# Kernel optimization log

Hardware: AMD Instinct MI355X
Metric: run time of the kernel (lower is better)

The kernel has to match this reference:

```python
import jax, jax.numpy as jnp
import numpy as np

N = 50000
E = 800000
IN_FEATS = 256
HIDDEN = 512
N_CLASSES = 40


def setup_inputs() -> dict:
    key = jax.random.key(0)
    ks = jax.random.split(key, 12)
    x = jax.random.normal(ks[0], (N, IN_FEATS), dtype=jnp.float32)
    src = jax.random.randint(ks[1], (E,), 0, N, dtype=jnp.int32)
    dst = jax.random.randint(ks[2], (E,), 0, N, dtype=jnp.int32)
    def glorot(k, fan_in, fan_out):
        lim = jnp.sqrt(6.0 / (fan_in + fan_out)).astype(jnp.float32)
        return jax.random.uniform(k, (fan_in, fan_out), jnp.float32, -lim, lim)
    W1 = glorot(ks[3], IN_FEATS, HIDDEN); b1 = jnp.zeros((HIDDEN,), jnp.float32)
    W2 = glorot(ks[4], HIDDEN, HIDDEN);   b2 = jnp.zeros((HIDDEN,), jnp.float32)
    W3 = glorot(ks[5], HIDDEN, HIDDEN);   b3 = jnp.zeros((HIDDEN,), jnp.float32)
    W4 = glorot(ks[6], HIDDEN, N_CLASSES); b4 = jnp.zeros((N_CLASSES,), jnp.float32)
    return {"x": x, "src": src, "dst": dst,
            "W1": W1, "b1": b1, "W2": W2, "b2": b2,
            "W3": W3, "b3": b3, "W4": W4, "b4": b4}


def _deg_inv_sqrt(idx, n):
    deg = jax.ops.segment_sum(jnp.ones_like(idx, jnp.float32), idx, num_segments=n)
    return jnp.where(deg > 0, jax.lax.rsqrt(jnp.maximum(deg, 1.0)), 0.0)


def _graph_conv(h, W, b, src, dst, c_src, c_dst, activation):
    # DGL GraphConv, norm='both': out = D_in^{-1/2} A D_out^{-1/2} h W + b
    h = h @ W                      # [N, out] dense transform first (reduces edge traffic)
    m = (h * c_src[:, None])[src]  # [E, out] gathered, src-normalized messages
    agg = jax.ops.segment_sum(m, dst, num_segments=h.shape[0])  # [N, out]
    out = agg * c_dst[:, None] + b
    return activation(out) if activation is not None else out


def reference(x, src, dst, W1, b1, W2, b2, W3, b3, W4, b4):
    n = x.shape[0]
    c_src = _deg_inv_sqrt(src, n)  # out-degree^{-1/2}
    c_dst = _deg_inv_sqrt(dst, n)  # in-degree^{-1/2}
    h = _graph_conv(x, W1, b1, src, dst, c_src, c_dst, jax.nn.relu)
    h = _graph_conv(h, W2, b2, src, dst, c_src, c_dst, jax.nn.relu)
    # dropout is identity in eval mode
    h = _graph_conv(h, W3, b3, src, dst, c_src, c_dst, jax.nn.relu)
    h = _graph_conv(h, W4, b4, src, dst, c_src, c_dst, None)
    return h
```

## Files before the change

### kernel.cpp

```cpp
#include <hip/hip_runtime.h>
#include <hip/hip_bf16.h>


#define GCN_N 50000
#define GCN_E 800000

typedef unsigned short u16;
typedef __attribute__((ext_vector_type(4))) float f32x4;
typedef __attribute__((ext_vector_type(4))) _Float16 f16x4;
typedef __attribute__((ext_vector_type(8))) _Float16 f16x8;

__device__ __forceinline__ void gload_lds16(const void* g, void* l) {
  __builtin_amdgcn_global_load_lds((const __attribute__((address_space(1))) void*)g,
                                   (__attribute__((address_space(3))) void*)l, 16, 0, 0);
}


__global__ void hist_kernel(const int* __restrict__ src, const int* __restrict__ dst,
                            int* __restrict__ deg_src, int* __restrict__ deg_dst, int E) {
  int i = blockIdx.x * blockDim.x + threadIdx.x;
  if (i < E) {
    atomicAdd(&deg_src[src[i]], 1);
    atomicAdd(&deg_dst[dst[i]], 1);
  }
}

__global__ void cinv_kernel(const int* __restrict__ deg_src, const int* __restrict__ deg_dst,
                            float* __restrict__ c_src, float* __restrict__ c_dst, int n) {
  int i = blockIdx.x * blockDim.x + threadIdx.x;
  if (i < n) {
    int ds = deg_src[i];
    int dd = deg_dst[i];
    c_src[i] = ds > 0 ? 1.0f / sqrtf((float)ds) : 0.0f;
    c_dst[i] = dd > 0 ? 1.0f / sqrtf((float)dd) : 0.0f;
  }
}

__global__ void scan_kernel(const int* __restrict__ deg, int* __restrict__ row_ptr,
                            int* __restrict__ cursor, int n) {
  __shared__ int wsum[16];
  __shared__ int s_carry;
  int lane = threadIdx.x & 63;
  int wid = threadIdx.x >> 6;
  if (threadIdx.x == 0) s_carry = 0;
  __syncthreads();
  for (int base = 0; base < n; base += 1024) {
    int i = base + (int)threadIdx.x;
    int v = (i < n) ? deg[i] : 0;
    int x = v;
    #pragma unroll
    for (int off = 1; off < 64; off <<= 1) {
      int y = __shfl_up(x, off, 64);
      if (lane >= off) x += y;
    }
    if (lane == 63) wsum[wid] = x;
    __syncthreads();
    int woff = s_carry;
    for (int w = 0; w < wid; ++w) woff += wsum[w];
    int incl = woff + x;
    if (i < n) {
      row_ptr[i] = incl - v;
      cursor[i] = incl - v;
    }
    __syncthreads();
    if (threadIdx.x == 1023) s_carry = incl;
    __syncthreads();
  }
  if (threadIdx.x == 0) row_ptr[n] = s_carry;
}

__global__ void fill_csr_kernel(const int* __restrict__ src, const int* __restrict__ dst,
                                int* __restrict__ cursor, int* __restrict__ csr_src, int E) {
  int i = blockIdx.x * blockDim.x + threadIdx.x;
  if (i < E) {
    int slot = atomicAdd(&cursor[dst[i]], 1);
    csr_src[slot] = src[i];
  }
}


__global__ void f32_to_f16_kernel(const float* __restrict__ in, _Float16* __restrict__ out,
                                  long n4) {
  long i = (long)blockIdx.x * blockDim.x + threadIdx.x;
  long stride = (long)gridDim.x * blockDim.x;
  for (; i < n4; i += stride) {
    float4 v = ((const float4*)in)[i];
    f16x4 h;
    h.x = (_Float16)v.x; h.y = (_Float16)v.y; h.z = (_Float16)v.z; h.w = (_Float16)v.w;
    ((f16x4*)out)[i] = h;
  }
}

template <typename VT, int NE, int G>
__global__ void agg16_kernel(const _Float16* __restrict__ in, _Float16* __restrict__ out,
                             const int* __restrict__ row_ptr, const int* __restrict__ csr_src,
                             const float* __restrict__ c_src, const float* __restrict__ c_dst) {
  int d = blockIdx.x;
  int t = threadIdx.x;
  if (t >= G) return;
  int beg = row_ptr[d];
  int end = row_ptr[d + 1];
  const VT* inv = (const VT*)in;
  float acc[NE];
  #pragma unroll
  for (int e = 0; e < NE; ++e) acc[e] = 0.f;
  int s_cur = 0; float c_cur = 0.f;
  if (beg < end) { s_cur = csr_src[beg]; c_cur = c_src[s_cur]; }
  for (int k = beg; k < end; ++k) {
    int s_nxt = 0; float c_nxt = 0.f;
    if (k + 1 < end) { s_nxt = csr_src[k + 1]; c_nxt = c_src[s_nxt]; }
    VT v = inv[(size_t)s_cur * G + t];
    #pragma unroll
    for (int e = 0; e < NE; ++e) acc[e] = fmaf(c_cur, (float)v[e], acc[e]);
    s_cur = s_nxt; c_cur = c_nxt;
  }
  float cd = c_dst[d];
  VT o;
  #pragma unroll
  for (int e = 0; e < NE; ++e) o[e] = (_Float16)(acc[e] * cd);
  ((VT*)out)[(size_t)d * G + t] = o;
}

__global__ void agg40_kernel(const _Float16* __restrict__ in, float* __restrict__ out,
                             const int* __restrict__ row_ptr, const int* __restrict__ csr_src,
                             const float* __restrict__ c_src, const float* __restrict__ c_dst,
                             const float* __restrict__ bias) {
  int d = blockIdx.x;
  int t = threadIdx.x;
  if (t >= 10) return;
  int beg = row_ptr[d];
  int end = row_ptr[d + 1];
  const f16x4* in4 = (const f16x4*)in;
  float ax = 0.f, ay = 0.f, az = 0.f, aw = 0.f;
  int s_cur = 0; float c_cur = 0.f;
  if (beg < end) { s_cur = csr_src[beg]; c_cur = c_src[s_cur]; }
  for (int k = beg; k < end; ++k) {
    int s_nxt = 0; float c_nxt = 0.f;
    if (k + 1 < end) { s_nxt = csr_src[k + 1]; c_nxt = c_src[s_nxt]; }
    f16x4 v = in4[(size_t)s_cur * 10 + t];
    ax = fmaf(c_cur, (float)v.x, ax);
    ay = fmaf(c_cur, (float)v.y, ay);
    az = fmaf(c_cur, (float)v.z, az);
    aw = fmaf(c_cur, (float)v.w, aw);
    s_cur = s_nxt; c_cur = c_nxt;
  }
  float cd = c_dst[d];
  float4 b = ((const float4*)bias)[t];
  float4 o;
  o.x = ax * cd + b.x;
  o.y = ay * cd + b.y;
  o.z = az * cd + b.z;
  o.w = aw * cd + b.w;
  ((float4*)out)[(size_t)d * 10 + t] = o;
}


__global__ void prep_weight_kernel(const float* __restrict__ W, _Float16* __restrict__ th,
                                   _Float16* __restrict__ tl, int K, int N) {
  __shared__ float tile[32][33];
  int bn = blockIdx.x * 32, bk = blockIdx.y * 32;
  int tx = threadIdx.x, ty = threadIdx.y;
  #pragma unroll
  for (int i = 0; i < 4; ++i)
    tile[ty + i * 8][tx] = W[(size_t)(bk + ty + i * 8) * N + bn + tx];
  __syncthreads();
  #pragma unroll
  for (int i = 0; i < 4; ++i) {
    float v = tile[tx][ty + i * 8];
    _Float16 h = (_Float16)v;
    _Float16 l = (_Float16)((v - (float)h) * 4096.f);
    size_t o = (size_t)(bn + ty + i * 8) * K + bk + tx;
    th[o] = h;
    tl[o] = l;
  }
}

__global__ __launch_bounds__(512, 4) void mfma_gemm_kernel(
    const _Float16* __restrict__ A,
    const _Float16* __restrict__ Bh, const _Float16* __restrict__ Bl,
    const float* __restrict__ bias, _Float16* __restrict__ C,
    int M, int K, int N) {
  __shared__ _Float16 sA[128 * 32], sBh[128 * 32], sBl[128 * 32];
  int t = threadIdx.x;
  int lane = t & 63, wid = t >> 6;
  int wr = wid >> 2, wc = wid & 3;
  int lr = lane & 15, ko = lane >> 4;
  int swz = (lr & 3) ^ ((lr >> 2) & 3);
  int koff = ((ko ^ swz) << 3);
  int bm = blockIdx.x * 128, bn = blockIdx.y * 128;

  f32x4 acch[4][2] = {};
  f32x4 accl[4][2] = {};

  int aoff[4], boff[2];
  #pragma unroll
  for (int i = 0; i < 4; ++i) aoff[i] = (wr * 64 + i * 16 + lr) * 32 + koff;
  #pragma unroll
  for (int j = 0; j < 2; ++j) boff[j] = (wc * 32 + j * 16 + lr) * 32 + koff;

  int srow = t >> 2;
  int sc = (t & 3) ^ ((srow & 3) ^ ((srow >> 2) & 3));
  int ldst = wid * 512;
  int gra = bm + srow;
  if (gra >= M) gra = M - 1;
  size_t gabase = (size_t)gra * K + sc * 8;
  size_t gbbase = (size_t)(bn + srow) * K + sc * 8;

  for (int k0 = 0; k0 < K; k0 += 32) {
    gload_lds16(A + gabase + k0, sA + ldst);
    gload_lds16(Bh + gbbase + k0, sBh + ldst);
    gload_lds16(Bl + gbbase + k0, sBl + ldst);
    __syncthreads();
    f16x8 a[4], bh[2], bl[2];
    #pragma unroll
    for (int i = 0; i < 4; ++i) a[i] = *(const f16x8*)(sA + aoff[i]);
    #pragma unroll
    for (int j = 0; j < 2; ++j) {
      bh[j] = *(const f16x8*)(sBh + boff[j]);
      bl[j] = *(const f16x8*)(sBl + boff[j]);
    }
    #pragma unroll
    for (int i = 0; i < 4; ++i)
      #pragma unroll
      for (int j = 0; j < 2; ++j) {
        acch[i][j] = __builtin_amdgcn_mfma_f32_16x16x32_f16(a[i], bh[j], acch[i][j], 0, 0, 0);
        accl[i][j] = __builtin_amdgcn_mfma_f32_16x16x32_f16(a[i], bl[j], accl[i][j], 0, 0, 0);
      }
    __syncthreads();
  }

  const float inv_s = 1.0f / 4096.0f;
  int r0 = (lane >> 4) << 2;
  #pragma unroll
  for (int i = 0; i < 4; ++i) {
    #pragma unroll
    for (int j = 0; j < 2; ++j) {
      int col = bn + wc * 32 + j * 16 + lr;
      float bv = bias[col];
      #pragma unroll
      for (int r = 0; r < 4; ++r) {
        int row = bm + wr * 64 + i * 16 + r0 + r;
        if (row < M) {
          float v = acch[i][j][r] + accl[i][j][r] * inv_s + bv;
          v = v > 0.f ? v : 0.f;
          C[(size_t)row * N + col] = (_Float16)v;
        }
      }
    }
  }
}


__global__ __launch_bounds__(256) void gemm40_kernel(const _Float16* __restrict__ A,
                                                     const float* __restrict__ W,
                                                     _Float16* __restrict__ C,
                                                     int M, int K, int N) {
  __shared__ float As[16][128 + 4];
  __shared__ float Bs[16][128 + 4];
  int tid = threadIdx.x;
  int tx = tid & 15;
  int ty = tid >> 4;
  int bm = blockIdx.x * 128;
  int bn = blockIdx.y * 128;

  float acc[8][8];
  #pragma unroll
  for (int i = 0; i < 8; ++i)
    #pragma unroll
    for (int j = 0; j < 8; ++j) acc[i][j] = 0.f;

  int ar = tid >> 2;
  int akq = (tid & 3) << 2;
  int bkk = tid >> 4;
  int bcq = (tid & 15) << 2;

  for (int k0 = 0; k0 < K; k0 += 16) {
    #pragma unroll
    for (int half = 0; half < 2; ++half) {
      int r = ar + half * 64;
      int grow = bm + r;
      float4 v = make_float4(0.f, 0.f, 0.f, 0.f);
      if (grow < M) {
        f16x4 hv = *(const f16x4*)&A[(size_t)grow * K + k0 + akq];
        v = make_float4((float)hv.x, (float)hv.y, (float)hv.z, (float)hv.w);
      }
      As[akq + 0][r] = v.x;
      As[akq + 1][r] = v.y;
      As[akq + 2][r] = v.z;
      As[akq + 3][r] = v.w;
    }
    #pragma unroll
    for (int half = 0; half < 2; ++half) {
      int c = bcq + half * 64;
      int gc = bn + c;
      float4 v = make_float4(0.f, 0.f, 0.f, 0.f);
      if (gc + 3 < N) v = *(const float4*)&W[(size_t)(k0 + bkk) * N + gc];
      *(float4*)&Bs[bkk][c] = v;
    }
    __syncthreads();
    #pragma unroll
    for (int kk = 0; kk < 16; ++kk) {
      float4 a0 = *(const float4*)&As[kk][ty * 4];
      float4 a1 = *(const float4*)&As[kk][ty * 4 + 64];
      float4 b0 = *(const float4*)&Bs[kk][tx * 4];
      float4 b1 = *(const float4*)&Bs[kk][tx * 4 + 64];
      float a[8] = {a0.x, a0.y, a0.z, a0.w, a1.x, a1.y, a1.z, a1.w};
      float b[8] = {b0.x, b0.y, b0.z, b0.w, b1.x, b1.y, b1.z, b1.w};
      #pragma unroll
      for (int i = 0; i < 8; ++i)
        #pragma unroll
        for (int j = 0; j < 8; ++j) acc[i][j] = fmaf(a[i], b[j], acc[i][j]);
    }
    __syncthreads();
  }

  #pragma unroll
  for (int i = 0; i < 8; ++i) {
    int r = bm + (i < 4 ? ty * 4 + i : 64 + ty * 4 + (i - 4));
    if (r >= M) continue;
    #pragma unroll
    for (int j = 0; j < 8; ++j) {
      int c = bn + (j < 4 ? tx * 4 + j : 64 + tx * 4 + (j - 4));
      if (c >= N) continue;
      C[(size_t)r * N + c] = (_Float16)acc[i][j];
    }
  }
}


extern "C" void kernel_launch(void* const* d_in, const int* in_sizes, int n_in,
                              void* d_out, int out_size, void* d_ws, size_t ws_size,
                              hipStream_t stream) {
  const float* x  = (const float*)d_in[0];
  const int* src  = (const int*)d_in[1];
  const int* dst  = (const int*)d_in[2];
  const float* W1 = (const float*)d_in[3];
  const float* b1 = (const float*)d_in[4];
  const float* W2 = (const float*)d_in[5];
  const float* b2 = (const float*)d_in[6];
  const float* W3 = (const float*)d_in[7];
  const float* b3 = (const float*)d_in[8];
  const float* W4 = (const float*)d_in[9];
  const float* b4 = (const float*)d_in[10];
  float* out = (float*)d_out;

  const int N = GCN_N, E = GCN_E;

  char* ws = (char*)d_ws;
  size_t off = 0;
  _Float16* h16a = (_Float16*)(ws + off); off += (size_t)N * 512 * 2;
  _Float16* h16b = (_Float16*)(ws + off); off += (size_t)N * 512 * 2;
  _Float16* x16  = (_Float16*)(ws + off); off += (size_t)N * 256 * 2;
  float* c_src = (float*)(ws + off); off += (size_t)N * 4;
  float* c_dst = (float*)(ws + off); off += (size_t)N * 4;
  int* row_ptr = (int*)(ws + off); off += (size_t)(N + 4) * 4;
  int* csr_src = (int*)(ws + off); off += (size_t)E * 4;
  _Float16* WtH1 = (_Float16*)(ws + off); off += (size_t)512 * 256 * 2;
  _Float16* WtL1 = (_Float16*)(ws + off); off += (size_t)512 * 256 * 2;
  _Float16* WtH2 = (_Float16*)(ws + off); off += (size_t)512 * 512 * 2;
  _Float16* WtL2 = (_Float16*)(ws + off); off += (size_t)512 * 512 * 2;
  _Float16* WtH3 = (_Float16*)(ws + off); off += (size_t)512 * 512 * 2;
  _Float16* WtL3 = (_Float16*)(ws + off); off += (size_t)512 * 512 * 2;
  int* deg_src = (int*)h16a;
  int* deg_dst = deg_src + N;
  int* cursor  = deg_dst + N;
  _Float16* t4 = x16;

  hipMemsetAsync(deg_src, 0, (size_t)2 * N * 4, stream);
  hist_kernel<<<(E + 255) / 256, 256, 0, stream>>>(src, dst, deg_src, deg_dst, E);
  cinv_kernel<<<(N + 255) / 256, 256, 0, stream>>>(deg_src, deg_dst, c_src, c_dst, N);
  scan_kernel<<<1, 1024, 0, stream>>>(deg_dst, row_ptr, cursor, N);
  fill_csr_kernel<<<(E + 255) / 256, 256, 0, stream>>>(src, dst, cursor, csr_src, E);

  prep_weight_kernel<<<dim3(16, 8), dim3(32, 8), 0, stream>>>(W1, WtH1, WtL1, 256, 512);
  prep_weight_kernel<<<dim3(16, 16), dim3(32, 8), 0, stream>>>(W2, WtH2, WtL2, 512, 512);
  prep_weight_kernel<<<dim3(16, 16), dim3(32, 8), 0, stream>>>(W3, WtH3, WtL3, 512, 512);

  f32_to_f16_kernel<<<2048, 256, 0, stream>>>(x, x16, (long)N * 256 / 4);

  int gm = (N + 127) / 128;

  agg16_kernel<f16x4, 4, 64><<<N, 64, 0, stream>>>(x16, h16a, row_ptr, csr_src, c_src, c_dst);
  mfma_gemm_kernel<<<dim3(gm, 4), 512, 0, stream>>>(h16a, WtH1, WtL1, b1, h16b, N, 256, 512);
  agg16_kernel<f16x8, 8, 64><<<N, 64, 0, stream>>>(h16b, h16a, row_ptr, csr_src, c_src, c_dst);
  mfma_gemm_kernel<<<dim3(gm, 4), 512, 0, stream>>>(h16a, WtH2, WtL2, b2, h16b, N, 512, 512);
  agg16_kernel<f16x8, 8, 64><<<N, 64, 0, stream>>>(h16b, h16a, row_ptr, csr_src, c_src, c_dst);
  mfma_gemm_kernel<<<dim3(gm, 4), 512, 0, stream>>>(h16a, WtH3, WtL3, b3, h16b, N, 512, 512);
  gemm40_kernel<<<dim3(gm, 1), 256, 0, stream>>>(h16b, W4, t4, N, 512, 40);
  agg40_kernel<<<N, 64, 0, stream>>>(t4, out, row_ptr, csr_src, c_src, c_dst, b4);
}
```

Before: 961.9 us.

## Parallelize CSR prefix scan across blocks and deepen gather prefetch in aggregation

Replaces the single-block 1024-thread serial-chunk scan over 50k degrees with a three-kernel reduce/scan/downsweep over 196 blocks, cutting a long serial prologue kernel. The aggregation kernels now prefetch two neighbor feature rows ahead instead of only the next index, keeping more gather loads in flight per thread. This adds two extra kernel launches and extra registers in the aggregation loops.

```diff
diff --git a/kernel.cpp b/kernel.cpp
--- a/kernel.cpp
+++ b/kernel.cpp
@@ -36,37 +36,57 @@
   }
 }
 
-__global__ void scan_kernel(const int* __restrict__ deg, int* __restrict__ row_ptr,
-                            int* __restrict__ cursor, int n) {
-  __shared__ int wsum[16];
-  __shared__ int s_carry;
+__device__ __forceinline__ int block_incl_scan(int v, int* lds) {
   int lane = threadIdx.x & 63;
   int wid = threadIdx.x >> 6;
-  if (threadIdx.x == 0) s_carry = 0;
+  int x = v;
+  #pragma unroll
+  for (int o = 1; o < 64; o <<= 1) {
+    int y = __shfl_up(x, o, 64);
+    if (lane >= o) x += y;
+  }
+  if (lane == 63) lds[wid] = x;
   __syncthreads();
-  for (int base = 0; base < n; base += 1024) {
-    int i = base + (int)threadIdx.x;
-    int v = (i < n) ? deg[i] : 0;
-    int x = v;
-    #pragma unroll
-    for (int off = 1; off < 64; off <<= 1) {
-      int y = __shfl_up(x, off, 64);
-      if (lane >= off) x += y;
-    }
-    if (lane == 63) wsum[wid] = x;
-    __syncthreads();
-    int woff = s_carry;
-    for (int w = 0; w < wid; ++w) woff += wsum[w];
-    int incl = woff + x;
-    if (i < n) {
-      row_ptr[i] = incl - v;
-      cursor[i] = incl - v;
-    }
-    __syncthreads();
-    if (threadIdx.x == 1023) s_carry = incl;
-    __syncthreads();
-  }
-  if (threadIdx.x == 0) row_ptr[n] = s_carry;
+  int off = 0;
+  #pragma unroll
+  for (int w = 0; w < 4; ++w)
+    if (w < wid) off += lds[w];
+  return x + off;
+}
+
+__global__ void deg_partial_kernel(const int* __restrict__ deg, int* __restrict__ partials, int n) {
+  __shared__ int lds[4];
+  int i = blockIdx.x * 256 + threadIdx.x;
+  int v = (i < n) ? deg[i] : 0;
+  int x = v;
+  #pragma unroll
+  for (int o = 1; o < 64; o <<= 1) x += __shfl_xor(x, o, 64);
+  if ((threadIdx.x & 63) == 0) lds[threadIdx.x >> 6] = x;
+  __syncthreads();
+  if (threadIdx.x == 0) partials[blockIdx.x] = lds[0] + lds[1] + lds[2] + lds[3];
+}
+
+__global__ void scan_partials_kernel(int* __restrict__ partials, int* __restrict__ row_ptr,
+                                     int nb, int n) {
+  __shared__ int lds[4];
+  int t = threadIdx.x;
+  int v = (t < nb) ? partials[t] : 0;
+  int incl = block_incl_scan(v, lds);
+  if (t < nb) partials[t] = incl - v;
+  if (t == 255) row_ptr[n] = incl;
+}
+
+__global__ void final_scan_kernel(const int* __restrict__ deg, const int* __restrict__ partials,
+                                  int* __restrict__ row_ptr, int* __restrict__ cursor, int n) {
+  __shared__ int lds[4];
+  int i = blockIdx.x * 256 + threadIdx.x;
+  int v = (i < n) ? deg[i] : 0;
+  int incl = block_incl_scan(v, lds);
+  int excl = incl - v + partials[blockIdx.x];
+  if (i < n) {
+    row_ptr[i] = excl;
+    cursor[i] = excl;
+  }
 }
 
 __global__ void fill_csr_kernel(const int* __restrict__ src, const int* __restrict__ dst,
@@ -99,20 +119,24 @@
   int t = threadIdx.x;
   if (t >= G) return;
   int beg = row_ptr[d];
-  int end = row_ptr[d + 1];
+  int cnt = row_ptr[d + 1] - beg;
   const VT* inv = (const VT*)in;
   float acc[NE];
   #pragma unroll
   for (int e = 0; e < NE; ++e) acc[e] = 0.f;
-  int s_cur = 0; float c_cur = 0.f;
-  if (beg < end) { s_cur = csr_src[beg]; c_cur = c_src[s_cur]; }
-  for (int k = beg; k < end; ++k) {
-    int s_nxt = 0; float c_nxt = 0.f;
-    if (k + 1 < end) { s_nxt = csr_src[k + 1]; c_nxt = c_src[s_nxt]; }
-    VT v = inv[(size_t)s_cur * G + t];
-    #pragma unroll
-    for (int e = 0; e < NE; ++e) acc[e] = fmaf(c_cur, (float)v[e], acc[e]);
-    s_cur = s_nxt; c_cur = c_nxt;
+
+  VT vA{}, vB{};
+  float cA = 0.f, cB = 0.f;
+  if (cnt > 0) { int s = csr_src[beg];     cA = c_src[s]; vA = inv[(size_t)s * G + t]; }
+  if (cnt > 1) { int s = csr_src[beg + 1]; cB = c_src[s]; vB = inv[(size_t)s * G + t]; }
+  for (int k = 0; k < cnt; ++k) {
+    VT vN{};
+    float cN = 0.f;
+    if (k + 2 < cnt) { int s = csr_src[beg + k + 2]; cN = c_src[s]; vN = inv[(size_t)s * G + t]; }
+    #pragma unroll
+    for (int e = 0; e < NE; ++e) acc[e] = fmaf(cA, (float)vA[e], acc[e]);
+    vA = vB; cA = cB;
+    vB = vN; cB = cN;
   }
   float cd = c_dst[d];
   VT o;
@@ -129,20 +153,24 @@
   int t = threadIdx.x;
   if (t >= 10) return;
   int beg = row_ptr[d];
-  int end = row_ptr[d + 1];
+  int cnt = row_ptr[d + 1] - beg;
   const f16x4* in4 = (const f16x4*)in;
   float ax = 0.f, ay = 0.f, az = 0.f, aw = 0.f;
-  int s_cur = 0; float c_cur = 0.f;
-  if (beg < end) { s_cur = csr_src[beg]; c_cur = c_src[s_cur]; }
-  for (int k = beg; k < end; ++k) {
-    int s_nxt = 0; float c_nxt = 0.f;
-    if (k + 1 < end) { s_nxt = csr_src[k + 1]; c_nxt = c_src[s_nxt]; }
-    f16x4 v = in4[(size_t)s_cur * 10 + t];
-    ax = fmaf(c_cur, (float)v.x, ax);
-    ay = fmaf(c_cur, (float)v.y, ay);
-    az = fmaf(c_cur, (float)v.z, az);
-    aw = fmaf(c_cur, (float)v.w, aw);
-    s_cur = s_nxt; c_cur = c_nxt;
+
+  f16x4 vA{}, vB{};
+  float cA = 0.f, cB = 0.f;
+  if (cnt > 0) { int s = csr_src[beg];     cA = c_src[s]; vA = in4[(size_t)s * 10 + t]; }
+  if (cnt > 1) { int s = csr_src[beg + 1]; cB = c_src[s]; vB = in4[(size_t)s * 10 + t]; }
+  for (int k = 0; k < cnt; ++k) {
+    f16x4 vN{};
+    float cN = 0.f;
+    if (k + 2 < cnt) { int s = csr_src[beg + k + 2]; cN = c_src[s]; vN = in4[(size_t)s * 10 + t]; }
+    ax = fmaf(cA, (float)vA.x, ax);
+    ay = fmaf(cA, (float)vA.y, ay);
+    az = fmaf(cA, (float)vA.z, az);
+    aw = fmaf(cA, (float)vA.w, aw);
+    vA = vB; cA = cB;
+    vB = vN; cB = cN;
   }
   float cd = c_dst[d];
   float4 b = ((const float4*)bias)[t];
@@ -345,6 +373,7 @@
   float* out = (float*)d_out;
 
   const int N = GCN_N, E = GCN_E;
+  const int NB = (N + 255) / 256;
 
   char* ws = (char*)d_ws;
   size_t off = 0;
@@ -355,6 +384,7 @@
   float* c_dst = (float*)(ws + off); off += (size_t)N * 4;
   int* row_ptr = (int*)(ws + off); off += (size_t)(N + 4) * 4;
   int* csr_src = (int*)(ws + off); off += (size_t)E * 4;
+  int* partials = (int*)(ws + off); off += 256 * 4;
   _Float16* WtH1 = (_Float16*)(ws + off); off += (size_t)512 * 256 * 2;
   _Float16* WtL1 = (_Float16*)(ws + off); off += (size_t)512 * 256 * 2;
   _Float16* WtH2 = (_Float16*)(ws + off); off += (size_t)512 * 512 * 2;
@@ -369,7 +399,9 @@
   hipMemsetAsync(deg_src, 0, (size_t)2 * N * 4, stream);
   hist_kernel<<<(E + 255) / 256, 256, 0, stream>>>(src, dst, deg_src, deg_dst, E);
   cinv_kernel<<<(N + 255) / 256, 256, 0, stream>>>(deg_src, deg_dst, c_src, c_dst, N);
-  scan_kernel<<<1, 1024, 0, stream>>>(deg_dst, row_ptr, cursor, N);
+  deg_partial_kernel<<<NB, 256, 0, stream>>>(deg_dst, partials, N);
+  scan_partials_kernel<<<1, 256, 0, stream>>>(partials, row_ptr, NB, N);
+  final_scan_kernel<<<NB, 256, 0, stream>>>(deg_dst, partials, row_ptr, cursor, N);
   fill_csr_kernel<<<(E + 255) / 256, 256, 0, stream>>>(src, dst, cursor, csr_src, E);
 
   prep_weight_kernel<<<dim3(16, 8), dim3(32, 8), 0, stream>>>(W1, WtH1, WtL1, 256, 512);
```

Result: faster. 911.6 us (-5.2%).
